# Optimization experiments

Hardware: AMD Instinct MI355X
Metric: run time of the kernel (lower is better)

Reference implementation:

```python
import jax, jax.numpy as jnp
import numpy as np

B, C, H, W = 4, 256, 64, 64
C8 = C // 8


def _xavier(key, shape):
    fan_in, fan_out = shape[1], shape[0]
    limit = float(np.sqrt(6.0 / (fan_in + fan_out)))
    return jax.random.uniform(key, shape, jnp.float32, -limit, limit)


def setup_inputs() -> dict:
    key = jax.random.key(0)
    ks = jax.random.split(key, 10)
    inp = {
        "x": jax.random.normal(ks[0], (B, C, H, W), jnp.float32),
        "y": jax.random.normal(ks[1], (B, C, H, W), jnp.float32),
        "Wfx": _xavier(ks[2], (C8, C)), "bfx": jnp.zeros((C8,), jnp.float32),
        "Wgx": _xavier(ks[3], (C8, C)), "bgx": jnp.zeros((C8,), jnp.float32),
        "Whx": _xavier(ks[4], (C, C)),  "bhx": jnp.zeros((C,), jnp.float32),
        "Wfy": _xavier(ks[5], (C8, C)), "bfy": jnp.zeros((C8,), jnp.float32),
        "Wgy": _xavier(ks[6], (C8, C)), "bgy": jnp.zeros((C8,), jnp.float32),
        "Why": _xavier(ks[7], (C, C)),  "bhy": jnp.zeros((C,), jnp.float32),
        # torch init is gamma=0 which zeroes the attention branch; use a random
        # scalar so the reference exercises the full computation.
        "gamma": jax.random.normal(ks[8], (1,), jnp.float32),
    }
    return inp


def _conv1x1(x, Wt, b):
    # 1x1 conv == per-pixel linear over channels; output flattened to [B, O, N]
    b_, c, h, w = x.shape
    out = jnp.einsum('oc,bchw->bohw', Wt, x) + b[None, :, None, None]
    return out.reshape(b_, -1, h * w)


def reference(x, y, Wfx, bfx, Wgx, bgx, Whx, bhx, Wfy, bfy, Wgy, bgy, Why, bhy, gamma):
    b, c, h, w = x.shape
    fx = _conv1x1(x, Wfx, bfx)  # [B, C8, N]
    gx = _conv1x1(x, Wgx, bgx)
    hx = _conv1x1(x, Whx, bhx)  # [B, C, N]
    fy = _conv1x1(y, Wfy, bfy)
    gy = _conv1x1(y, Wgy, bgy)
    hy = _conv1x1(y, Why, bhy)

    # attention_x = softmax(f_y^T @ g_x) over last dim; [B, N, N]
    att_x = jax.nn.softmax(jnp.einsum('bcn,bcm->bnm', fy, gx), axis=-1)
    att_y = jax.nn.softmax(jnp.einsum('bcn,bcm->bnm', fx, gy), axis=-1)

    sa_x = jnp.einsum('bcn,bnm->bcm', hx, att_x).reshape(b, c, h, w)
    sa_y = jnp.einsum('bcn,bnm->bcm', hy, att_y).reshape(b, c, h, w)

    out_x = gamma[0] * sa_x + x
    out_y = gamma[0] * sa_y + y
    return (out_x, out_y)
```

## Files before the change

### kernel.cpp

```cpp
#include <hip/hip_runtime.h>

#define BB 4
#define CC 256
#define NN 4096

typedef _Float16 half_t;
typedef __attribute__((ext_vector_type(8))) _Float16 half8;
typedef __attribute__((ext_vector_type(4))) _Float16 half4;
typedef __attribute__((ext_vector_type(4))) float floatx4;
typedef __attribute__((ext_vector_type(16))) float floatx16;

__global__ __launch_bounds__(256)
void cvt_w_kernel(const float* __restrict__ Wfx, const float* __restrict__ Wgx,
                  const float* __restrict__ Whx, const float* __restrict__ Wfy,
                  const float* __restrict__ Wgy, const float* __restrict__ Why,
                  half_t* __restrict__ oWfx, half_t* __restrict__ oWgx,
                  half_t* __restrict__ oWhx, half_t* __restrict__ oWfy,
                  half_t* __restrict__ oWgy, half_t* __restrict__ oWhy)
{
    const float* src; half_t* dst; int n;
    switch (blockIdx.y) {
        case 0: src = Wfx; dst = oWfx; n = 32 * CC; break;
        case 1: src = Wgx; dst = oWgx; n = 32 * CC; break;
        case 2: src = Whx; dst = oWhx; n = CC * CC; break;
        case 3: src = Wfy; dst = oWfy; n = 32 * CC; break;
        case 4: src = Wgy; dst = oWgy; n = 32 * CC; break;
        default: src = Why; dst = oWhy; n = CC * CC; break;
    }
    int idx = (blockIdx.x * 256 + threadIdx.x) * 4;
    if (idx >= n) return;
    float4 v = *(const float4*)&src[idx];
    half4 h; h[0] = (half_t)v.x; h[1] = (half_t)v.y; h[2] = (half_t)v.z; h[3] = (half_t)v.w;
    *(half4*)&dst[idx] = h;
}

__global__ __launch_bounds__(256)
void transpose_cvt_kernel(const float* __restrict__ x, const float* __restrict__ y,
                          half_t* __restrict__ xTx, half_t* __restrict__ xTy)
{
    const int n0 = blockIdx.x * 64;
    const int c0 = blockIdx.y * 64;
    const int b  = blockIdx.z & 3;
    const int sel = blockIdx.z >> 2;
    const float* in = sel ? y : x;
    half_t* outT = sel ? xTy : xTx;
    const int t  = threadIdx.x;
    const int ch = t & 7, nl = t >> 3;
    const float* inb = in + (size_t)b * CC * NN;
    half_t* outb = outT + (size_t)b * NN * CC;

    #pragma unroll
    for (int p = 0; p < 2; ++p) {
        int n = n0 + nl + 32 * p;
        half8 hv;
        #pragma unroll
        for (int j = 0; j < 8; ++j)
            hv[j] = (half_t)inb[(size_t)(c0 + 8 * ch + j) * NN + n];
        *(half8*)&outb[(size_t)n * CC + c0 + 8 * ch] = hv;
    }
}

__global__ __launch_bounds__(256)
void proj_fg_kernel(const half_t* __restrict__ xTx, const half_t* __restrict__ xTy,
                    const half_t* __restrict__ Wfx, const half_t* __restrict__ Wgx,
                    const half_t* __restrict__ Wfy, const half_t* __restrict__ Wgy,
                    const float* __restrict__ bfx, const float* __restrict__ bgx,
                    const float* __restrict__ bfy, const float* __restrict__ bgy,
                    half_t* __restrict__ fxT, half_t* __restrict__ gxT,
                    half_t* __restrict__ fyT, half_t* __restrict__ gyT)
{
    const int n0 = blockIdx.x * 64;
    const int b  = blockIdx.y;
    const int sel = blockIdx.z;
    const half_t* xT = sel ? xTy : xTx;
    const half_t* Wf = sel ? Wfy : Wfx;
    const half_t* Wg = sel ? Wgy : Wgx;
    const float*  bf = sel ? bfy : bfx;
    const float*  bg = sel ? bgy : bgx;
    half_t* fT = sel ? fyT : fxT;
    half_t* gT = sel ? gyT : gxT;

    const int t  = threadIdx.x;
    const int w = t >> 6, lane = t & 63, q = lane >> 4, mc = lane & 15;
    const half_t* xTb = xT + (size_t)b * NN * CC;

    floatx4 acc[4];
    #pragma unroll
    for (int i = 0; i < 4; ++i) {
        float bv = (i < 2 ? bf : bg)[(i & 1) * 16 + mc];
        acc[i] = (floatx4){bv, bv, bv, bv};
    }

    #pragma unroll
    for (int ks = 0; ks < 8; ++ks) {
        int k0 = ks * 32 + q * 8;
        half8 af = *(const half8*)&xTb[(size_t)(n0 + w * 16 + mc) * CC + k0];
        #pragma unroll
        for (int i = 0; i < 4; ++i) {
            const half_t* Ws = (i < 2) ? Wf : Wg;
            half8 bfr = *(const half8*)&Ws[(size_t)((i & 1) * 16 + mc) * CC + k0];
            acc[i] = __builtin_amdgcn_mfma_f32_16x16x32_f16(af, bfr, acc[i], 0, 0, 0);
        }
    }

    #pragma unroll
    for (int i = 0; i < 4; ++i) {
        half_t* dst = (i < 2) ? fT : gT;
        #pragma unroll
        for (int r = 0; r < 4; ++r) {
            int n = n0 + w * 16 + q * 4 + r;
            dst[((size_t)b * NN + n) * 32 + (i & 1) * 16 + mc] = (half_t)acc[i][r];
        }
    }
}

__global__ __launch_bounds__(256)
void proj_h_kernel(const half_t* __restrict__ xTx, const half_t* __restrict__ xTy,
                   const half_t* __restrict__ Whx, const half_t* __restrict__ Why,
                   const float* __restrict__ bhx, const float* __restrict__ bhy,
                   half_t* __restrict__ hx, half_t* __restrict__ hy)
{
    const int n0 = blockIdx.x * 64;
    const int o0 = blockIdx.y * 128;
    const int b  = blockIdx.z & 3;
    const int sel = blockIdx.z >> 2;
    const half_t* xT = sel ? xTy : xTx;
    const half_t* Wh = sel ? Why : Whx;
    const float*  bh = sel ? bhy : bhx;
    half_t* h = sel ? hy : hx;

    const int t  = threadIdx.x;
    const int w = t >> 6, lane = t & 63, q = lane >> 4, mc = lane & 15;
    const half_t* xTb = xT + (size_t)b * NN * CC;
    half_t* hb = h + (size_t)b * CC * NN;

    floatx4 acc[2][4];
    #pragma unroll
    for (int j = 0; j < 2; ++j) {
        floatx4 bv;
        #pragma unroll
        for (int r = 0; r < 4; ++r) bv[r] = bh[o0 + w * 32 + j * 16 + q * 4 + r];
        #pragma unroll
        for (int i = 0; i < 4; ++i) acc[j][i] = bv;
    }

    #pragma unroll
    for (int ks = 0; ks < 8; ++ks) {
        int k0 = ks * 32 + q * 8;
        half8 a0 = *(const half8*)&Wh[(size_t)(o0 + w * 32 + mc) * CC + k0];
        half8 a1 = *(const half8*)&Wh[(size_t)(o0 + w * 32 + 16 + mc) * CC + k0];
        #pragma unroll
        for (int i = 0; i < 4; ++i) {
            half8 bfr = *(const half8*)&xTb[(size_t)(n0 + i * 16 + mc) * CC + k0];
            acc[0][i] = __builtin_amdgcn_mfma_f32_16x16x32_f16(a0, bfr, acc[0][i], 0, 0, 0);
            acc[1][i] = __builtin_amdgcn_mfma_f32_16x16x32_f16(a1, bfr, acc[1][i], 0, 0, 0);
        }
    }

    #pragma unroll
    for (int j = 0; j < 2; ++j)
        #pragma unroll
        for (int i = 0; i < 4; ++i)
            #pragma unroll
            for (int r = 0; r < 4; ++r) {
                int o = o0 + w * 32 + j * 16 + q * 4 + r;
                hb[(size_t)o * NN + n0 + i * 16 + mc] = (half_t)acc[j][i][r];
            }
}

__global__ __launch_bounds__(256)
void stats_kernel(const half_t* __restrict__ fT0, const half_t* __restrict__ gT0,
                  const half_t* __restrict__ fT1, const half_t* __restrict__ gT1,
                  float* __restrict__ L0, float* __restrict__ L1)
{
    __shared__ float red_l[4][32];
    const int b  = blockIdx.y;
    const int sel = blockIdx.z;
    const half_t* fT = sel ? fT1 : fT0;
    const half_t* gT = sel ? gT1 : gT0;
    float* Lout = sel ? L1 : L0;

    const int n0 = blockIdx.x * 32;
    const int t  = threadIdx.x;
    const int w = t >> 6, lane = t & 63, q = lane >> 4, mc = lane & 15;
    const half_t* fTb = fT + (size_t)b * NN * 32;
    const half_t* gTb = gT + (size_t)b * NN * 32;

    half8 a0 = *(const half8*)&fTb[(size_t)(n0 + mc) * 32 + q * 8];
    half8 a1 = *(const half8*)&fTb[(size_t)(n0 + 16 + mc) * 32 + q * 8];

    float l0[4] = {0.f, 0.f, 0.f, 0.f}, l1[4] = {0.f, 0.f, 0.f, 0.f};
    for (int it = 0; it < NN / 64; ++it) {
        int m = (it * 4 + w) * 16 + mc;
        half8 bfr = *(const half8*)&gTb[(size_t)m * 32 + q * 8];
        floatx4 S0 = __builtin_amdgcn_mfma_f32_16x16x32_f16(a0, bfr, (floatx4){0.f,0.f,0.f,0.f}, 0, 0, 0);
        floatx4 S1 = __builtin_amdgcn_mfma_f32_16x16x32_f16(a1, bfr, (floatx4){0.f,0.f,0.f,0.f}, 0, 0, 0);
        #pragma unroll
        for (int r = 0; r < 4; ++r) { l0[r] += __expf(S0[r]); l1[r] += __expf(S1[r]); }
    }
    #pragma unroll
    for (int r = 0; r < 4; ++r) {
        #pragma unroll
        for (int off = 1; off < 16; off <<= 1) {
            l0[r] += __shfl_xor(l0[r], off);
            l1[r] += __shfl_xor(l1[r], off);
        }
    }
    if (mc == 0)
        #pragma unroll
        for (int r = 0; r < 4; ++r) {
            red_l[w][q * 4 + r]      = l0[r];
            red_l[w][16 + q * 4 + r] = l1[r];
        }
    __syncthreads();
    if (t < 32) {
        float L = red_l[0][t] + red_l[1][t] + red_l[2][t] + red_l[3][t];
        Lout[(size_t)b * NN + n0 + t] = -log2f(L);
    }
}

__global__ __launch_bounds__(256)
void pv_kernel(const half_t* __restrict__ fT0, const half_t* __restrict__ gT0,
               const half_t* __restrict__ h0, const float* __restrict__ L0,
               const float* __restrict__ src0, float* __restrict__ out0,
               const half_t* __restrict__ fT1, const half_t* __restrict__ gT1,
               const half_t* __restrict__ h1, const float* __restrict__ L1,
               const float* __restrict__ src1, float* __restrict__ out1,
               const float* __restrict__ gamma)
{
    __shared__ half_t h_lds[128][72];
    __shared__ half_t PT[128][72];

    const int m0 = blockIdx.x * 128;
    const int c0 = blockIdx.y * 128;
    const int b  = blockIdx.z & 3;
    const int sel = blockIdx.z >> 2;
    const half_t* fT = sel ? fT1 : fT0;
    const half_t* gT = sel ? gT1 : gT0;
    const half_t* h  = sel ? h1 : h0;
    const float*  Lg = sel ? L1 : L0;
    const float*  src = sel ? src1 : src0;
    float* out = sel ? out1 : out0;

    const int t = threadIdx.x;
    const int w = t >> 6, lane = t & 63;
    const int q = lane >> 4, mc = lane & 15;
    const int l5 = lane >> 5, l31 = lane & 31;

    const half_t* fTb = fT + (size_t)b * NN * 32;
    const half_t* gTb = gT + (size_t)b * NN * 32;
    const half_t* hb  = h + (size_t)b * CC * NN;
    const float*  Lb  = Lg + (size_t)b * NN;

    half8 gS[2];
    gS[0] = *(const half8*)&gTb[(size_t)(m0 + w * 32 + mc) * 32 + q * 8];
    gS[1] = *(const half8*)&gTb[(size_t)(m0 + w * 32 + 16 + mc) * 32 + q * 8];

    const int srow = t >> 3;
    const int sch  = t & 7;

    half8 hpre[4], fpre[4];
    #pragma unroll
    for (int i = 0; i < 4; ++i)
        hpre[i] = *(const half8*)&hb[(size_t)(c0 + srow + 32 * i) * NN + sch * 8];
    #pragma unroll
    for (int s = 0; s < 4; ++s)
        fpre[s] = *(const half8*)&fTb[(size_t)(s * 16 + mc) * 32 + q * 8];

    floatx16 acc[2][2];
    #pragma unroll
    for (int a = 0; a < 2; ++a)
        #pragma unroll
        for (int bm = 0; bm < 2; ++bm)
            #pragma unroll
            for (int r = 0; r < 16; ++r) acc[a][bm][r] = 0.f;

    const int ca = (w >> 1) * 64;
    const int mb = (w & 1) * 64;

    for (int nt = 0; nt < NN; nt += 64) {
        __syncthreads();
        #pragma unroll
        for (int i = 0; i < 4; ++i)
            *(half8*)&h_lds[srow + 32 * i][sch * 8] = hpre[i];

        #pragma unroll
        for (int s = 0; s < 4; ++s) {
            float4 lv = *(const float4*)&Lb[nt + s * 16 + q * 4];
            #pragma unroll
            for (int u = 0; u < 2; ++u) {
                floatx4 S = __builtin_amdgcn_mfma_f32_16x16x32_f16(
                    fpre[s], gS[u], (floatx4){0.f, 0.f, 0.f, 0.f}, 0, 0, 0);
                half4 p;
                p[0] = (half_t)exp2f(fmaf(S[0], 1.44269504f, lv.x));
                p[1] = (half_t)exp2f(fmaf(S[1], 1.44269504f, lv.y));
                p[2] = (half_t)exp2f(fmaf(S[2], 1.44269504f, lv.z));
                p[3] = (half_t)exp2f(fmaf(S[3], 1.44269504f, lv.w));
                *(half4*)&PT[w * 32 + u * 16 + mc][s * 16 + q * 4] = p;
            }
        }
        __syncthreads();

        int ntn = nt + 64; if (ntn >= NN) ntn = 0;
        #pragma unroll
        for (int i = 0; i < 4; ++i)
            hpre[i] = *(const half8*)&hb[(size_t)(c0 + srow + 32 * i) * NN + ntn + sch * 8];
        #pragma unroll
        for (int s = 0; s < 4; ++s)
            fpre[s] = *(const half8*)&fTb[(size_t)(ntn + s * 16 + mc) * 32 + q * 8];

        #pragma unroll
        for (int ch = 0; ch < 4; ++ch) {
            half8 B0 = *(const half8*)&PT[mb + l31][ch * 16 + l5 * 8];
            half8 B1 = *(const half8*)&PT[mb + 32 + l31][ch * 16 + l5 * 8];
            half8 A0 = *(const half8*)&h_lds[ca + l31][ch * 16 + l5 * 8];
            half8 A1 = *(const half8*)&h_lds[ca + 32 + l31][ch * 16 + l5 * 8];
            acc[0][0] = __builtin_amdgcn_mfma_f32_32x32x16_f16(A0, B0, acc[0][0], 0, 0, 0);
            acc[0][1] = __builtin_amdgcn_mfma_f32_32x32x16_f16(A0, B1, acc[0][1], 0, 0, 0);
            acc[1][0] = __builtin_amdgcn_mfma_f32_32x32x16_f16(A1, B0, acc[1][0], 0, 0, 0);
            acc[1][1] = __builtin_amdgcn_mfma_f32_32x32x16_f16(A1, B1, acc[1][1], 0, 0, 0);
        }
    }

    const float gm = gamma[0];
    const float* srcb = src + (size_t)b * CC * NN;
    float* outb = out + (size_t)b * CC * NN;
    #pragma unroll
    for (int a = 0; a < 2; ++a)
        #pragma unroll
        for (int bm = 0; bm < 2; ++bm) {
            const int m = m0 + mb + bm * 32 + l31;
            #pragma unroll
            for (int r = 0; r < 16; ++r) {
                int c = c0 + ca + a * 32 + (r & 3) + 8 * (r >> 2) + 4 * l5;
                size_t idx = (size_t)c * NN + m;
                outb[idx] = fmaf(gm, acc[a][bm][r], srcb[idx]);
            }
        }
}

extern "C" void kernel_launch(void* const* d_in, const int* in_sizes, int n_in,
                              void* d_out, int out_size, void* d_ws, size_t ws_size,
                              hipStream_t stream)
{
    const float* x   = (const float*)d_in[0];
    const float* y   = (const float*)d_in[1];
    const float* Wfx = (const float*)d_in[2];
    const float* bfx = (const float*)d_in[3];
    const float* Wgx = (const float*)d_in[4];
    const float* bgx = (const float*)d_in[5];
    const float* Whx = (const float*)d_in[6];
    const float* bhx = (const float*)d_in[7];
    const float* Wfy = (const float*)d_in[8];
    const float* bfy = (const float*)d_in[9];
    const float* Wgy = (const float*)d_in[10];
    const float* bgy = (const float*)d_in[11];
    const float* Why = (const float*)d_in[12];
    const float* bhy = (const float*)d_in[13];
    const float* gam = (const float*)d_in[14];

    const size_t SZ_XT = (size_t)BB * NN * CC;
    const size_t SZ_FG = (size_t)BB * NN * 32;
    half_t* xTx   = (half_t*)d_ws;
    half_t* xTy   = xTx + SZ_XT;
    half_t* hx    = xTy + SZ_XT;
    half_t* hy    = hx + SZ_XT;
    half_t* fxT   = hy + SZ_XT;
    half_t* gxT   = fxT + SZ_FG;
    half_t* fyT   = gxT + SZ_FG;
    half_t* gyT   = fyT + SZ_FG;
    half_t* Wfx_h = gyT + SZ_FG;
    half_t* Wgx_h = Wfx_h + 32 * CC;
    half_t* Wfy_h = Wgx_h + 32 * CC;
    half_t* Wgy_h = Wfy_h + 32 * CC;
    half_t* Whx_h = Wgy_h + 32 * CC;
    half_t* Why_h = Whx_h + CC * CC;
    float*  Lx    = (float*)(Why_h + CC * CC);
    float*  Ly    = Lx + (size_t)BB * NN;

    float* outx = (float*)d_out;
    float* outy = outx + (size_t)BB * CC * NN;

    cvt_w_kernel<<<dim3(64, 6), 256, 0, stream>>>(Wfx, Wgx, Whx, Wfy, Wgy, Why,
                                                  Wfx_h, Wgx_h, Whx_h, Wfy_h, Wgy_h, Why_h);

    transpose_cvt_kernel<<<dim3(64, 4, 8), 256, 0, stream>>>(x, y, xTx, xTy);

    proj_fg_kernel<<<dim3(64, 4, 2), 256, 0, stream>>>(
        xTx, xTy, Wfx_h, Wgx_h, Wfy_h, Wgy_h, bfx, bgx, bfy, bgy, fxT, gxT, fyT, gyT);

    proj_h_kernel<<<dim3(64, 2, 8), 256, 0, stream>>>(
        xTx, xTy, Whx_h, Why_h, bhx, bhy, hx, hy);

    stats_kernel<<<dim3(128, 4, 2), 256, 0, stream>>>(fyT, gxT, fxT, gyT, Lx, Ly);

    pv_kernel<<<dim3(32, 2, 8), 256, 0, stream>>>(
        fyT, gxT, hx, Lx, x, outx,
        fxT, gyT, hy, Ly, y, outy, gam);
}
```

Baseline: 306.7 us.

## Double-buffer pv_kernel LDS with XOR swizzle and 512-thread blocks

pv_kernel now runs 512 threads (8 waves) per block. Each wave owns 16 query columns for the score/exp step and a 64x32 output tile, which halves the per-wave accumulator count and recomputation of P. The h and P tiles are double-buffered in LDS so only one barrier per iteration is needed. Padding is replaced by an XOR swizzle to avoid bank conflicts. The aim is better latency hiding and overlap between the exp work and the PV MFMAs, at the cost of more LDS and a register cap set by launch bounds (512, 4).

```diff
diff --git a/kernel.cpp b/kernel.cpp
--- a/kernel.cpp
+++ b/kernel.cpp
@@ -219,7 +219,7 @@
     }
 }
 
-__global__ __launch_bounds__(256)
+__global__ __launch_bounds__(512, 4)
 void pv_kernel(const half_t* __restrict__ fT0, const half_t* __restrict__ gT0,
                const half_t* __restrict__ h0, const float* __restrict__ L0,
                const float* __restrict__ src0, float* __restrict__ out0,
@@ -228,8 +228,8 @@
                const float* __restrict__ src1, float* __restrict__ out1,
                const float* __restrict__ gamma)
 {
-    __shared__ half_t h_lds[128][72];
-    __shared__ half_t PT[128][72];
+    __shared__ half_t h_lds[2][128][64];
+    __shared__ half_t PT[2][128][64];
 
     const int m0 = blockIdx.x * 128;
     const int c0 = blockIdx.y * 128;
@@ -252,90 +252,99 @@
     const half_t* hb  = h + (size_t)b * CC * NN;
     const float*  Lb  = Lg + (size_t)b * NN;
 
-    half8 gS[2];
-    gS[0] = *(const half8*)&gTb[(size_t)(m0 + w * 32 + mc) * 32 + q * 8];
-    gS[1] = *(const half8*)&gTb[(size_t)(m0 + w * 32 + 16 + mc) * 32 + q * 8];
-
-    const int srow = t >> 3;
-    const int sch  = t & 7;
-
-    half8 hpre[4], fpre[4];
-    #pragma unroll
-    for (int i = 0; i < 4; ++i)
-        hpre[i] = *(const half8*)&hb[(size_t)(c0 + srow + 32 * i) * NN + sch * 8];
-    #pragma unroll
-    for (int s = 0; s < 4; ++s)
-        fpre[s] = *(const half8*)&fTb[(size_t)(s * 16 + mc) * 32 + q * 8];
-
-    floatx16 acc[2][2];
+    const half8 gS = *(const half8*)&gTb[(size_t)(m0 + w * 16 + mc) * 32 + q * 8];
+
+    const int sj = t & 7;
+    const int sr = t >> 3;
+    const int sjx = sj ^ (sr & 7);
+
+    const int ca = (w >> 2) * 64;
+    const int mb = (w & 3) * 32;
+    const int swzr = l31 & 7;
+
+    floatx16 acc[2];
     #pragma unroll
     for (int a = 0; a < 2; ++a)
         #pragma unroll
-        for (int bm = 0; bm < 2; ++bm)
-            #pragma unroll
-            for (int r = 0; r < 16; ++r) acc[a][bm][r] = 0.f;
-
-    const int ca = (w >> 1) * 64;
-    const int mb = (w & 1) * 64;
-
-    for (int nt = 0; nt < NN; nt += 64) {
+        for (int r = 0; r < 16; ++r) acc[a][r] = 0.f;
+
+    {
+        half8 hg0 = *(const half8*)&hb[(size_t)(c0 + sr) * NN + sjx * 8];
+        half8 hg1 = *(const half8*)&hb[(size_t)(c0 + sr + 64) * NN + sjx * 8];
+        half8 af[4]; float4 lv[4];
+        #pragma unroll
+        for (int s = 0; s < 4; ++s) {
+            af[s] = *(const half8*)&fTb[(size_t)(s * 16 + mc) * 32 + q * 8];
+            lv[s] = *(const float4*)&Lb[s * 16 + q * 4];
+        }
+        *(half8*)&h_lds[0][sr][sj * 8]      = hg0;
+        *(half8*)&h_lds[0][sr + 64][sj * 8] = hg1;
+        #pragma unroll
+        for (int s = 0; s < 4; ++s) {
+            floatx4 S = __builtin_amdgcn_mfma_f32_16x16x32_f16(
+                af[s], gS, (floatx4){0.f, 0.f, 0.f, 0.f}, 0, 0, 0);
+            half4 p;
+            p[0] = (half_t)exp2f(fmaf(S[0], 1.44269504f, lv[s].x));
+            p[1] = (half_t)exp2f(fmaf(S[1], 1.44269504f, lv[s].y));
+            p[2] = (half_t)exp2f(fmaf(S[2], 1.44269504f, lv[s].z));
+            p[3] = (half_t)exp2f(fmaf(S[3], 1.44269504f, lv[s].w));
+            *(half4*)&PT[0][w * 16 + mc]
+                [(((2 * s + (q >> 1)) ^ (mc & 7)) << 3) + ((q & 1) << 2)] = p;
+        }
+    }
+    __syncthreads();
+
+    for (int it = 0; it < NN / 64; ++it) {
+        const int cur = it & 1, nxt = cur ^ 1;
+        int ntn = (it + 1) * 64; if (ntn >= NN) ntn = 0;
+
+        half8 hg0 = *(const half8*)&hb[(size_t)(c0 + sr) * NN + ntn + sjx * 8];
+        half8 hg1 = *(const half8*)&hb[(size_t)(c0 + sr + 64) * NN + ntn + sjx * 8];
+        half8 af[4]; float4 lv[4];
+        #pragma unroll
+        for (int s = 0; s < 4; ++s) {
+            af[s] = *(const half8*)&fTb[(size_t)(ntn + s * 16 + mc) * 32 + q * 8];
+            lv[s] = *(const float4*)&Lb[ntn + s * 16 + q * 4];
+        }
+
+        #pragma unroll
+        for (int ch = 0; ch < 4; ++ch) {
+            const int cidx = ((2 * ch + l5) ^ swzr) << 3;
+            half8 Bf = *(const half8*)&PT[cur][mb + l31][cidx];
+            half8 A0 = *(const half8*)&h_lds[cur][ca + l31][cidx];
+            half8 A1 = *(const half8*)&h_lds[cur][ca + 32 + l31][cidx];
+            acc[0] = __builtin_amdgcn_mfma_f32_32x32x16_f16(A0, Bf, acc[0], 0, 0, 0);
+            acc[1] = __builtin_amdgcn_mfma_f32_32x32x16_f16(A1, Bf, acc[1], 0, 0, 0);
+        }
+
+        *(half8*)&h_lds[nxt][sr][sj * 8]      = hg0;
+        *(half8*)&h_lds[nxt][sr + 64][sj * 8] = hg1;
+        #pragma unroll
+        for (int s = 0; s < 4; ++s) {
+            floatx4 S = __builtin_amdgcn_mfma_f32_16x16x32_f16(
+                af[s], gS, (floatx4){0.f, 0.f, 0.f, 0.f}, 0, 0, 0);
+            half4 p;
+            p[0] = (half_t)exp2f(fmaf(S[0], 1.44269504f, lv[s].x));
+            p[1] = (half_t)exp2f(fmaf(S[1], 1.44269504f, lv[s].y));
+            p[2] = (half_t)exp2f(fmaf(S[2], 1.44269504f, lv[s].z));
+            p[3] = (half_t)exp2f(fmaf(S[3], 1.44269504f, lv[s].w));
+            *(half4*)&PT[nxt][w * 16 + mc]
+                [(((2 * s + (q >> 1)) ^ (mc & 7)) << 3) + ((q & 1) << 2)] = p;
+        }
         __syncthreads();
-        #pragma unroll
-        for (int i = 0; i < 4; ++i)
-            *(half8*)&h_lds[srow + 32 * i][sch * 8] = hpre[i];
-
-        #pragma unroll
-        for (int s = 0; s < 4; ++s) {
-            float4 lv = *(const float4*)&Lb[nt + s * 16 + q * 4];
-            #pragma unroll
-            for (int u = 0; u < 2; ++u) {
-                floatx4 S = __builtin_amdgcn_mfma_f32_16x16x32_f16(
-                    fpre[s], gS[u], (floatx4){0.f, 0.f, 0.f, 0.f}, 0, 0, 0);
-                half4 p;
-                p[0] = (half_t)exp2f(fmaf(S[0], 1.44269504f, lv.x));
-                p[1] = (half_t)exp2f(fmaf(S[1], 1.44269504f, lv.y));
-                p[2] = (half_t)exp2f(fmaf(S[2], 1.44269504f, lv.z));
-                p[3] = (half_t)exp2f(fmaf(S[3], 1.44269504f, lv.w));
-                *(half4*)&PT[w * 32 + u * 16 + mc][s * 16 + q * 4] = p;
-            }
-        }
-        __syncthreads();
-
-        int ntn = nt + 64; if (ntn >= NN) ntn = 0;
-        #pragma unroll
-        for (int i = 0; i < 4; ++i)
-            hpre[i] = *(const half8*)&hb[(size_t)(c0 + srow + 32 * i) * NN + ntn + sch * 8];
-        #pragma unroll
-        for (int s = 0; s < 4; ++s)
-            fpre[s] = *(const half8*)&fTb[(size_t)(ntn + s * 16 + mc) * 32 + q * 8];
-
-        #pragma unroll
-        for (int ch = 0; ch < 4; ++ch) {
-            half8 B0 = *(const half8*)&PT[mb + l31][ch * 16 + l5 * 8];
-            half8 B1 = *(const half8*)&PT[mb + 32 + l31][ch * 16 + l5 * 8];
-            half8 A0 = *(const half8*)&h_lds[ca + l31][ch * 16 + l5 * 8];
-            half8 A1 = *(const half8*)&h_lds[ca + 32 + l31][ch * 16 + l5 * 8];
-            acc[0][0] = __builtin_amdgcn_mfma_f32_32x32x16_f16(A0, B0, acc[0][0], 0, 0, 0);
-            acc[0][1] = __builtin_amdgcn_mfma_f32_32x32x16_f16(A0, B1, acc[0][1], 0, 0, 0);
-            acc[1][0] = __builtin_amdgcn_mfma_f32_32x32x16_f16(A1, B0, acc[1][0], 0, 0, 0);
-            acc[1][1] = __builtin_amdgcn_mfma_f32_32x32x16_f16(A1, B1, acc[1][1], 0, 0, 0);
-        }
     }
 
     const float gm = gamma[0];
     const float* srcb = src + (size_t)b * CC * NN;
     float* outb = out + (size_t)b * CC * NN;
+    const int m = m0 + mb + l31;
     #pragma unroll
     for (int a = 0; a < 2; ++a)
         #pragma unroll
-        for (int bm = 0; bm < 2; ++bm) {
-            const int m = m0 + mb + bm * 32 + l31;
-            #pragma unroll
-            for (int r = 0; r < 16; ++r) {
-                int c = c0 + ca + a * 32 + (r & 3) + 8 * (r >> 2) + 4 * l5;
-                size_t idx = (size_t)c * NN + m;
-                outb[idx] = fmaf(gm, acc[a][bm][r], srcb[idx]);
-            }
+        for (int r = 0; r < 16; ++r) {
+            int c = c0 + ca + a * 32 + (r & 3) + 8 * (r >> 2) + 4 * l5;
+            size_t idx = (size_t)c * NN + m;
+            outb[idx] = fmaf(gm, acc[a][r], srcb[idx]);
         }
 }
 
@@ -394,7 +403,7 @@
 
     stats_kernel<<<dim3(128, 4, 2), 256, 0, stream>>>(fyT, gxT, fxT, gyT, Lx, Ly);
 
-    pv_kernel<<<dim3(32, 2, 8), 256, 0, stream>>>(
+    pv_kernel<<<dim3(32, 2, 8), 512, 0, stream>>>(
         fyT, gxT, hx, Lx, x, outx,
         fxT, gyT, hy, Ly, y, outy, gam);
 }
```

Measured after the change: 314.6 us. +2.6%, slower.

## Retile PV kernel to cover all channels per block, removing recomputed exp

Applied to the files above, without the earlier changes.

The PV kernel now uses 512-thread blocks, each covering all 256 channels for 64 output positions. Before, each block covered 128 channels by 128 positions, so the QK^T scores and exp for every position were computed twice, once per channel half. The new tiling computes each probability tile once per block and shares it across all 8 waves. The trade-offs are a smaller P tile per block, less MFMA work per wave, a larger h tile in LDS, and register pressure from the occupancy hint in launch_bounds.

```diff
diff --git a/kernel.cpp b/kernel.cpp
--- a/kernel.cpp
+++ b/kernel.cpp
@@ -219,7 +219,7 @@
     }
 }
 
-__global__ __launch_bounds__(256)
+__global__ __launch_bounds__(512, 4)
 void pv_kernel(const half_t* __restrict__ fT0, const half_t* __restrict__ gT0,
                const half_t* __restrict__ h0, const float* __restrict__ L0,
                const float* __restrict__ src0, float* __restrict__ out0,
@@ -228,13 +228,12 @@
                const float* __restrict__ src1, float* __restrict__ out1,
                const float* __restrict__ gamma)
 {
-    __shared__ half_t h_lds[128][72];
-    __shared__ half_t PT[128][72];
-
-    const int m0 = blockIdx.x * 128;
-    const int c0 = blockIdx.y * 128;
-    const int b  = blockIdx.z & 3;
-    const int sel = blockIdx.z >> 2;
+    __shared__ half_t h_lds[256][72];
+    __shared__ half_t PT[64][72];
+
+    const int m0 = blockIdx.x * 64;
+    const int b  = blockIdx.y & 3;
+    const int sel = blockIdx.y >> 2;
     const half_t* fT = sel ? fT1 : fT0;
     const half_t* gT = sel ? gT1 : gT0;
     const half_t* h  = sel ? h1 : h0;
@@ -247,78 +246,71 @@
     const int q = lane >> 4, mc = lane & 15;
     const int l5 = lane >> 5, l31 = lane & 31;
 
+    const int mg  = (w >> 1) * 16;
+    const int nhf = (w & 1) * 32;
+
     const half_t* fTb = fT + (size_t)b * NN * 32;
     const half_t* gTb = gT + (size_t)b * NN * 32;
     const half_t* hb  = h + (size_t)b * CC * NN;
     const float*  Lb  = Lg + (size_t)b * NN;
 
-    half8 gS[2];
-    gS[0] = *(const half8*)&gTb[(size_t)(m0 + w * 32 + mc) * 32 + q * 8];
-    gS[1] = *(const half8*)&gTb[(size_t)(m0 + w * 32 + 16 + mc) * 32 + q * 8];
+    const half8 gS = *(const half8*)&gTb[(size_t)(m0 + mg + mc) * 32 + q * 8];
 
     const int srow = t >> 3;
     const int sch  = t & 7;
 
-    half8 hpre[4], fpre[4];
+    half8 hpre[4]; half8 fpre[2]; float4 lv[2];
     #pragma unroll
     for (int i = 0; i < 4; ++i)
-        hpre[i] = *(const half8*)&hb[(size_t)(c0 + srow + 32 * i) * NN + sch * 8];
-    #pragma unroll
-    for (int s = 0; s < 4; ++s)
-        fpre[s] = *(const half8*)&fTb[(size_t)(s * 16 + mc) * 32 + q * 8];
-
-    floatx16 acc[2][2];
-    #pragma unroll
-    for (int a = 0; a < 2; ++a)
-        #pragma unroll
-        for (int bm = 0; bm < 2; ++bm)
-            #pragma unroll
-            for (int r = 0; r < 16; ++r) acc[a][bm][r] = 0.f;
-
-    const int ca = (w >> 1) * 64;
-    const int mb = (w & 1) * 64;
+        hpre[i] = *(const half8*)&hb[(size_t)(srow + 64 * i) * NN + sch * 8];
+    #pragma unroll
+    for (int s = 0; s < 2; ++s) {
+        fpre[s] = *(const half8*)&fTb[(size_t)(nhf + s * 16 + mc) * 32 + q * 8];
+        lv[s]   = *(const float4*)&Lb[nhf + s * 16 + q * 4];
+    }
+
+    floatx16 acc[2];
+    #pragma unroll
+    for (int bm = 0; bm < 2; ++bm)
+        #pragma unroll
+        for (int r = 0; r < 16; ++r) acc[bm][r] = 0.f;
 
     for (int nt = 0; nt < NN; nt += 64) {
         __syncthreads();
         #pragma unroll
         for (int i = 0; i < 4; ++i)
-            *(half8*)&h_lds[srow + 32 * i][sch * 8] = hpre[i];
-
-        #pragma unroll
-        for (int s = 0; s < 4; ++s) {
-            float4 lv = *(const float4*)&Lb[nt + s * 16 + q * 4];
-            #pragma unroll
-            for (int u = 0; u < 2; ++u) {
-                floatx4 S = __builtin_amdgcn_mfma_f32_16x16x32_f16(
-                    fpre[s], gS[u], (floatx4){0.f, 0.f, 0.f, 0.f}, 0, 0, 0);
-                half4 p;
-                p[0] = (half_t)exp2f(fmaf(S[0], 1.44269504f, lv.x));
-                p[1] = (half_t)exp2f(fmaf(S[1], 1.44269504f, lv.y));
-                p[2] = (half_t)exp2f(fmaf(S[2], 1.44269504f, lv.z));
-                p[3] = (half_t)exp2f(fmaf(S[3], 1.44269504f, lv.w));
-                *(half4*)&PT[w * 32 + u * 16 + mc][s * 16 + q * 4] = p;
-            }
+            *(half8*)&h_lds[srow + 64 * i][sch * 8] = hpre[i];
+
+        #pragma unroll
+        for (int s = 0; s < 2; ++s) {
+            floatx4 S = __builtin_amdgcn_mfma_f32_16x16x32_f16(
+                fpre[s], gS, (floatx4){0.f, 0.f, 0.f, 0.f}, 0, 0, 0);
+            half4 p;
+            p[0] = (half_t)exp2f(fmaf(S[0], 1.44269504f, lv[s].x));
+            p[1] = (half_t)exp2f(fmaf(S[1], 1.44269504f, lv[s].y));
+            p[2] = (half_t)exp2f(fmaf(S[2], 1.44269504f, lv[s].z));
+            p[3] = (half_t)exp2f(fmaf(S[3], 1.44269504f, lv[s].w));
+            *(half4*)&PT[mg + mc][nhf + s * 16 + q * 4] = p;
         }
         __syncthreads();
 
         int ntn = nt + 64; if (ntn >= NN) ntn = 0;
         #pragma unroll
         for (int i = 0; i < 4; ++i)
-            hpre[i] = *(const half8*)&hb[(size_t)(c0 + srow + 32 * i) * NN + ntn + sch * 8];
-        #pragma unroll
-        for (int s = 0; s < 4; ++s)
-            fpre[s] = *(const half8*)&fTb[(size_t)(ntn + s * 16 + mc) * 32 + q * 8];
+            hpre[i] = *(const half8*)&hb[(size_t)(srow + 64 * i) * NN + ntn + sch * 8];
+        #pragma unroll
+        for (int s = 0; s < 2; ++s) {
+            fpre[s] = *(const half8*)&fTb[(size_t)(ntn + nhf + s * 16 + mc) * 32 + q * 8];
+            lv[s]   = *(const float4*)&Lb[ntn + nhf + s * 16 + q * 4];
+        }
 
         #pragma unroll
         for (int ch = 0; ch < 4; ++ch) {
-            half8 B0 = *(const half8*)&PT[mb + l31][ch * 16 + l5 * 8];
-            half8 B1 = *(const half8*)&PT[mb + 32 + l31][ch * 16 + l5 * 8];
-            half8 A0 = *(const half8*)&h_lds[ca + l31][ch * 16 + l5 * 8];
-            half8 A1 = *(const half8*)&h_lds[ca + 32 + l31][ch * 16 + l5 * 8];
-            acc[0][0] = __builtin_amdgcn_mfma_f32_32x32x16_f16(A0, B0, acc[0][0], 0, 0, 0);
-            acc[0][1] = __builtin_amdgcn_mfma_f32_32x32x16_f16(A0, B1, acc[0][1], 0, 0, 0);
-            acc[1][0] = __builtin_amdgcn_mfma_f32_32x32x16_f16(A1, B0, acc[1][0], 0, 0, 0);
-            acc[1][1] = __builtin_amdgcn_mfma_f32_32x32x16_f16(A1, B1, acc[1][1], 0, 0, 0);
+            half8 Ah = *(const half8*)&h_lds[w * 32 + l31][ch * 16 + l5 * 8];
+            half8 B0 = *(const half8*)&PT[l31][ch * 16 + l5 * 8];
+            half8 B1 = *(const half8*)&PT[32 + l31][ch * 16 + l5 * 8];
+            acc[0] = __builtin_amdgcn_mfma_f32_32x32x16_f16(Ah, B0, acc[0], 0, 0, 0);
+            acc[1] = __builtin_amdgcn_mfma_f32_32x32x16_f16(Ah, B1, acc[1], 0, 0, 0);
         }
     }
 
@@ -326,17 +318,15 @@
     const float* srcb = src + (size_t)b * CC * NN;
     float* outb = out + (size_t)b * CC * NN;
     #pragma unroll
-    for (int a = 0; a < 2; ++a)
-        #pragma unroll
-        for (int bm = 0; bm < 2; ++bm) {
-            const int m = m0 + mb + bm * 32 + l31;
-            #pragma unroll
-            for (int r = 0; r < 16; ++r) {
-                int c = c0 + ca + a * 32 + (r & 3) + 8 * (r >> 2) + 4 * l5;
-                size_t idx = (size_t)c * NN + m;
-                outb[idx] = fmaf(gm, acc[a][bm][r], srcb[idx]);
-            }
-        }
+    for (int bm = 0; bm < 2; ++bm) {
+        const int m = m0 + bm * 32 + l31;
+        #pragma unroll
+        for (int r = 0; r < 16; ++r) {
+            int c = w * 32 + (r & 3) + 8 * (r >> 2) + 4 * l5;
+            size_t idx = (size_t)c * NN + m;
+            outb[idx] = fmaf(gm, acc[bm][r], srcb[idx]);
+        }
+    }
 }
 
 extern "C" void kernel_launch(void* const* d_in, const int* in_sizes, int n_in,
@@ -394,7 +384,7 @@
 
     stats_kernel<<<dim3(128, 4, 2), 256, 0, stream>>>(fyT, gxT, fxT, gyT, Lx, Ly);
 
-    pv_kernel<<<dim3(32, 2, 8), 256, 0, stream>>>(
+    pv_kernel<<<dim3(64, 8), 512, 0, stream>>>(
         fyT, gxT, hx, Lx, x, outx,
         fxT, gyT, hy, Ly, y, outy, gam);
 }
```

Measured after the change: 281.4 us. 8.2% less time.
